# Kernel optimization log

Hardware: AMD Instinct MI355X
Metric: run time of the kernel (lower is better)

## Reference

```python
import jax, jax.numpy as jnp
import numpy as np

N, E, B = 50000, 500000, 32
FEAT, HID, EDGE_DIM = 64, 128, 16
NUM_TASKS, TED, NCLS, TASKS_PER = 5000, 64, 3, 8
NLAYERS = 2


def setup_inputs() -> dict:
    key = jax.random.key(0)
    ks = jax.random.split(key, 20)
    s = 0.05
    inp = {
        "h": jax.random.normal(ks[0], (N, FEAT), jnp.float32),
        "x": jax.random.normal(ks[1], (N, 3), jnp.float32),
        "edge_index": jax.random.randint(ks[2], (2, E), 0, N, dtype=jnp.int32),
        "edge_attr": jax.random.normal(ks[3], (E, EDGE_DIM), jnp.float32),
        "batch": (jnp.arange(N, dtype=jnp.int32) * B // N).astype(jnp.int32),
        "tasks_indices": jnp.stack([
            jnp.repeat(jnp.arange(B, dtype=jnp.int32), TASKS_PER),
            jax.random.randint(ks[4], (B * TASKS_PER,), 0, NUM_TASKS, dtype=jnp.int32),
        ], axis=1),
        "batch_size": B,
        "embed_W": jax.random.normal(ks[5], (FEAT, HID), jnp.float32) * s,
        "embed_b": jnp.zeros((HID,), jnp.float32),
        "res_W": jax.random.normal(ks[6], (NLAYERS, HID, HID), jnp.float32) * s,
        "msg_W": jax.random.normal(ks[7], (NLAYERS, 2 * HID + 1, HID), jnp.float32) * s,
        "msg_b": jnp.zeros((NLAYERS, HID), jnp.float32),
        "upd_W": jax.random.normal(ks[8], (NLAYERS, 2 * HID, HID), jnp.float32) * s,
        "upd_b": jnp.zeros((NLAYERS, HID), jnp.float32),
        "mlp_W0": jax.random.normal(ks[9], (HID + TED, HID), jnp.float32) * s,
        "mlp_b0": jnp.zeros((HID,), jnp.float32),
        "mlp_W1": jax.random.normal(ks[10], (HID, HID), jnp.float32) * s,
        "mlp_b1": jnp.zeros((HID,), jnp.float32),
        "mlp_W2": jax.random.normal(ks[11], (HID, HID), jnp.float32) * s,
        "mlp_b2": jnp.zeros((HID,), jnp.float32),
        "mlp_W3": jax.random.normal(ks[12], (HID, NCLS), jnp.float32) * s,
        "mlp_b3": jnp.zeros((NCLS,), jnp.float32),
        "task_emb": jax.random.normal(ks[13], (NUM_TASKS, TED), jnp.float32),
    }
    return inp


def reference(h, x, edge_index, edge_attr, batch, tasks_indices, batch_size,
              embed_W, embed_b, res_W, msg_W, msg_b, upd_W, upd_b,
              mlp_W0, mlp_b0, mlp_W1, mlp_b1, mlp_W2, mlp_b2, mlp_W3, mlp_b3,
              task_emb):
    n = h.shape[0]
    row, col = edge_index[0], edge_index[1]
    # squared distances, identical across MP layers (positions never updated)
    dist = jnp.sum((x[row] - x[col]) ** 2, axis=1, keepdims=True)  # [E,1]
    emb = h @ embed_W + embed_b  # [N,HID]
    for l in range(NLAYERS):
        msg_in = jnp.concatenate([emb[row], emb[col], dist], axis=-1)  # [E,2H+1]
        msg = jax.nn.relu(msg_in @ msg_W[l] + msg_b[l])                # [E,H]
        aggr = jax.ops.segment_sum(msg, col, num_segments=n)           # [N,H]
        upd = jax.nn.relu(jnp.concatenate([emb, aggr], axis=-1) @ upd_W[l] + upd_b[l])
        emb = emb @ res_W[l] + upd
    # global mean pool per graph
    counts = jax.ops.segment_sum(jnp.ones((n,), emb.dtype), batch, num_segments=batch_size)
    pooled = jax.ops.segment_sum(emb, batch, num_segments=batch_size) / jnp.maximum(counts, 1.0)[:, None]
    # per-(protein, task) head; rows ordered as in the original dict-over-batch loop
    proto = tasks_indices[:, 0]
    tid = tasks_indices[:, 1]
    feat = jnp.concatenate([pooled[proto], task_emb[tid]], axis=-1)  # [K, H+TED]
    z = jax.nn.relu(feat @ mlp_W0 + mlp_b0)
    z = jax.nn.relu(z @ mlp_W1 + mlp_b1)
    z = jax.nn.relu(z @ mlp_W2 + mlp_b2)
    return z @ mlp_W3 + mlp_b3  # [K, NCLS]
```

## Files before the change

### kernel.cpp

```cpp
#include <hip/hip_runtime.h>

constexpr int NN = 50000;
constexpr int NE = 500000;
constexpr int NB = 32;
constexpr int NTROWS = 256;
constexpr int SCB = 196;
constexpr int NBLK64 = (NN + 63) / 64;

typedef __attribute__((ext_vector_type(8))) short bf16x8;
typedef __attribute__((ext_vector_type(4))) float f32x4;

static __device__ __forceinline__ unsigned short f2bf(float f) {
  unsigned u = __float_as_uint(f);
  unsigned r = (u + 0x7FFFu + ((u >> 16) & 1u)) >> 16;
  return (unsigned short)r;
}
static __device__ __forceinline__ float bf2f(unsigned short s) {
  return __uint_as_float(((unsigned)s) << 16);
}

__global__ void k_wprep(const float* __restrict__ msgW, const float* __restrict__ updW,
                        const float* __restrict__ resW, const float* __restrict__ embW,
                        unsigned short* __restrict__ wbf, int* __restrict__ cnt) {
  int idx = blockIdx.x * 256 + threadIdx.x;
  if (idx < NN) cnt[idx] = 0;
  if (idx >= 10 * 16384 + 8192) return;
  if (idx < 10 * 16384) {
    int m = idx >> 14, e = idx & 16383;
    int nn = e >> 7, kk = e & 127;
    int l = m / 5, t = m % 5;
    const float* src;
    if (t == 0)      src = msgW + (size_t)l * 257 * 128;
    else if (t == 1) src = msgW + (size_t)l * 257 * 128 + 128 * 128;
    else if (t == 2) src = updW + (size_t)l * 256 * 128;
    else if (t == 3) src = updW + (size_t)l * 256 * 128 + 128 * 128;
    else             src = resW + (size_t)l * 128 * 128;
    wbf[idx] = f2bf(src[kk * 128 + nn]);
  } else {
    int e = idx - 10 * 16384;
    int nn = e >> 6, kk = e & 63;
    wbf[idx] = f2bf(embW[kk * 128 + nn]);
  }
}

__global__ void k_count_gstart(const int* __restrict__ col, int* __restrict__ cnt,
                               const int* __restrict__ batch, int* __restrict__ gstart) {
  int e = blockIdx.x * 256 + threadIdx.x;
  if (e < NE) atomicAdd(&cnt[col[e]], 1);
  if (e < NN) {
    int b = batch[e];
    if (e == 0) gstart[b] = 0;
    else if (batch[e - 1] != b) gstart[b] = e;
    if (e == NN - 1) gstart[b + 1] = NN;
  }
}

__global__ __launch_bounds__(256) void k_scan1(const int* __restrict__ cnt,
                                               int* __restrict__ starts,
                                               int* __restrict__ bsum) {
  __shared__ int s[256];
  int t = threadIdx.x;
  int i = blockIdx.x * 256 + t;
  int v = (i < NN) ? cnt[i] : 0;
  s[t] = v; __syncthreads();
  for (int off = 1; off < 256; off <<= 1) {
    int u = (t >= off) ? s[t - off] : 0;
    __syncthreads();
    s[t] += u;
    __syncthreads();
  }
  if (i < NN) starts[i] = s[t] - v;
  if (t == 255) bsum[blockIdx.x] = s[255];
}

__global__ __launch_bounds__(256) void k_scan2(int* __restrict__ bsum) {
  __shared__ int s[256];
  int t = threadIdx.x;
  int v = (t < SCB) ? bsum[t] : 0;
  s[t] = v; __syncthreads();
  for (int off = 1; off < 256; off <<= 1) {
    int u = (t >= off) ? s[t - off] : 0;
    __syncthreads();
    s[t] += u;
    __syncthreads();
  }
  if (t < SCB) bsum[t] = s[t] - v;
}

__global__ __launch_bounds__(256) void k_scan3(int* __restrict__ starts,
                                               const int* __restrict__ bsum,
                                               int* __restrict__ cursor) {
  int i = blockIdx.x * 256 + threadIdx.x;
  if (i < NN) {
    int v = starts[i] + bsum[blockIdx.x];
    starts[i] = v;
    cursor[i] = v;
  }
  if (i == 0) starts[NN] = NE;
}

__global__ void k_scatter(const int* __restrict__ row, const int* __restrict__ col,
                          const float* __restrict__ x,
                          int* __restrict__ cursor, int2* __restrict__ spack) {
  int e = blockIdx.x * blockDim.x + threadIdx.x;
  if (e >= NE) return;
  int r = row[e], c = col[e];
  float dx = x[3*r+0] - x[3*c+0];
  float dy = x[3*r+1] - x[3*c+1];
  float dz = x[3*r+2] - x[3*c+2];
  float d = dx*dx + dy*dy + dz*dz;
  int pos = atomicAdd(&cursor[c], 1);
  spack[pos] = make_int2(r, __float_as_int(d));
}

template<int TPB>
static __device__ __forceinline__ void stage_tile64(
    unsigned short* lds, const unsigned short* __restrict__ src, int row0, int n, int tid) {
  #pragma unroll
  for (int ch = tid; ch < 1024; ch += TPB) {
    int r = ch >> 4, kc = ch & 15;
    bf16x8 v = {0,0,0,0,0,0,0,0};
    if (row0 + r < n) v = *(const bf16x8*)(src + (size_t)(row0 + r) * 128 + kc * 8);
    int byte = (r * 256 + kc * 16) ^ ((r & 7) << 4);
    *(bf16x8*)((char*)lds + byte) = v;
  }
}

template<int TPB>
static __device__ __forceinline__ void vstore_tile64(
    unsigned short* __restrict__ dst, const unsigned short* lds, int row0, int n, int tid) {
  #pragma unroll
  for (int ch = tid; ch < 1024; ch += TPB) {
    int r = ch >> 4, kc = ch & 15;
    if (row0 + r < n) {
      bf16x8 v = *(const bf16x8*)((const char*)lds + ((r * 256 + kc * 16) ^ ((r & 7) << 4)));
      *(bf16x8*)(dst + (size_t)(row0 + r) * 128 + kc * 8) = v;
    }
  }
}

static __device__ __forceinline__ void epi_to_lds64(
    unsigned short* lds, const f32x4 (&acc)[4], int lane, int c0) {
  int ccol = lane & 15, crow4 = (lane >> 4) * 4;
  int cc = c0 + ccol;
  #pragma unroll
  for (int rt = 0; rt < 4; ++rt)
    #pragma unroll
    for (int j = 0; j < 4; ++j) {
      int lrow = rt * 16 + crow4 + j;
      int lbyte = (lrow * 256 + cc * 2) ^ ((lrow & 7) << 4);
      *(unsigned short*)((char*)lds + lbyte) = f2bf(acc[rt][j]);
    }
}

static __device__ __forceinline__ void gather_aggr_lds(
    unsigned short* As, const int* __restrict__ starts, const int2* __restrict__ spack,
    const unsigned short* __restrict__ A, const unsigned short* __restrict__ Bm,
    const float* __restrict__ wd, const float* __restrict__ mb,
    int row0, int n, int tid) {
  int c0 = (tid & 15) * 8;
  float4 w0 = *(const float4*)(wd + c0), w1 = *(const float4*)(wd + c0 + 4);
  float4 bb0 = *(const float4*)(mb + c0), bb1 = *(const float4*)(mb + c0 + 4);
  float wv[8] = {w0.x, w0.y, w0.z, w0.w, w1.x, w1.y, w1.z, w1.w};
  float bv[8] = {bb0.x, bb0.y, bb0.z, bb0.w, bb1.x, bb1.y, bb1.z, bb1.w};
  #pragma unroll
  for (int pass = 0; pass < 2; ++pass) {
    int lr = (tid >> 4) + pass * 32;
    int node = row0 + lr;
    union { bf16x8 v; unsigned short s[8]; } o;
    if (node < n) {
      union { bf16x8 v; unsigned short s[8]; } ub;
      ub.v = *(const bf16x8*)(Bm + (size_t)node * 128 + c0);
      float basev[8], accv[8];
      #pragma unroll
      for (int j = 0; j < 8; ++j) { basev[j] = bf2f(ub.s[j]) + bv[j]; accv[j] = 0.f; }
      int s = starts[node], e = starts[node + 1];
      int i = s;
      for (; i + 4 <= e; i += 4) {
        int2 p0 = spack[i + 0], p1 = spack[i + 1];
        int2 p2 = spack[i + 2], p3 = spack[i + 3];
        union { bf16x8 v; unsigned short s[8]; } a0, a1, a2, a3;
        a0.v = *(const bf16x8*)(A + (size_t)p0.x * 128 + c0);
        a1.v = *(const bf16x8*)(A + (size_t)p1.x * 128 + c0);
        a2.v = *(const bf16x8*)(A + (size_t)p2.x * 128 + c0);
        a3.v = *(const bf16x8*)(A + (size_t)p3.x * 128 + c0);
        float d0 = __int_as_float(p0.y), d1 = __int_as_float(p1.y);
        float d2 = __int_as_float(p2.y), d3 = __int_as_float(p3.y);
        #pragma unroll
        for (int j = 0; j < 8; ++j) {
          accv[j] += fmaxf(bf2f(a0.s[j]) + fmaf(d0, wv[j], basev[j]), 0.f);
          accv[j] += fmaxf(bf2f(a1.s[j]) + fmaf(d1, wv[j], basev[j]), 0.f);
          accv[j] += fmaxf(bf2f(a2.s[j]) + fmaf(d2, wv[j], basev[j]), 0.f);
          accv[j] += fmaxf(bf2f(a3.s[j]) + fmaf(d3, wv[j], basev[j]), 0.f);
        }
      }
      for (; i < e; ++i) {
        int2 p = spack[i];
        union { bf16x8 v; unsigned short s[8]; } a;
        a.v = *(const bf16x8*)(A + (size_t)p.x * 128 + c0);
        float d = __int_as_float(p.y);
        #pragma unroll
        for (int j = 0; j < 8; ++j)
          accv[j] += fmaxf(bf2f(a.s[j]) + fmaf(d, wv[j], basev[j]), 0.f);
      }
      #pragma unroll
      for (int j = 0; j < 8; ++j) o.s[j] = f2bf(accv[j]);
    } else {
      #pragma unroll
      for (int j = 0; j < 8; ++j) o.s[j] = 0;
    }
    int byte = (lr * 256 + (tid & 15) * 16) ^ ((lr & 7) << 4);
    *(bf16x8*)((char*)As + byte) = o.v;
  }
}

__global__ __launch_bounds__(512) void k_embed_dual(
    const float* __restrict__ h, const unsigned short* __restrict__ embWt,
    const float* __restrict__ embB,
    const unsigned short* __restrict__ W1t, const unsigned short* __restrict__ W2t,
    unsigned short* __restrict__ emb, unsigned short* __restrict__ Y1,
    unsigned short* __restrict__ Y2, int n) {
  __shared__ unsigned short T0[64 * 128];
  __shared__ unsigned short T1[64 * 128];
  int row0 = blockIdx.x * 64;
  int tid = threadIdx.x;
  int wave = tid >> 6, lane = tid & 63;
  int c0 = wave * 16;
  int arow = lane & 15, kb = (lane >> 4) * 8;
  {
    int r = tid >> 3, kc = tid & 7;
    union { bf16x8 v; unsigned short s[8]; } u;
    if (row0 + r < n) {
      const float* p = h + (size_t)(row0 + r) * 64 + kc * 8;
      float4 f0 = *(const float4*)p, f1 = *(const float4*)(p + 4);
      u.s[0]=f2bf(f0.x); u.s[1]=f2bf(f0.y); u.s[2]=f2bf(f0.z); u.s[3]=f2bf(f0.w);
      u.s[4]=f2bf(f1.x); u.s[5]=f2bf(f1.y); u.s[6]=f2bf(f1.z); u.s[7]=f2bf(f1.w);
    } else {
      #pragma unroll
      for (int j = 0; j < 8; ++j) u.s[j] = 0;
    }
    int byte = (r * 128 + kc * 16) ^ ((r & 7) << 4);
    *(bf16x8*)((char*)T0 + byte) = u.v;
  }
  float bB = embB[c0 + (lane & 15)];
  __syncthreads();
  f32x4 accE[4] = {};
  #pragma unroll
  for (int ks = 0; ks < 2; ++ks) {
    bf16x8 b = *(const bf16x8*)(embWt + (size_t)(c0 + arow) * 64 + ks * 32 + kb);
    #pragma unroll
    for (int rt = 0; rt < 4; ++rt) {
      int r = rt * 16 + arow;
      int byte = (r * 128 + (ks * 32 + kb) * 2) ^ ((r & 7) << 4);
      bf16x8 a = *(const bf16x8*)((const char*)T0 + byte);
      accE[rt] = __builtin_amdgcn_mfma_f32_16x16x32_bf16(a, b, accE[rt], 0, 0, 0);
    }
  }
  {
    int ccol = lane & 15, crow4 = (lane >> 4) * 4;
    int cc = c0 + ccol;
    #pragma unroll
    for (int rt = 0; rt < 4; ++rt)
      #pragma unroll
      for (int j = 0; j < 4; ++j) {
        int lrow = rt * 16 + crow4 + j;
        int lbyte = (lrow * 256 + cc * 2) ^ ((lrow & 7) << 4);
        *(unsigned short*)((char*)T1 + lbyte) = f2bf(accE[rt][j] + bB);
      }
  }
  __syncthreads();
  f32x4 acc1[4] = {};
  f32x4 acc2[4] = {};
  #pragma unroll
  for (int ks = 0; ks < 4; ++ks) {
    int k0 = ks * 32;
    bf16x8 b1 = *(const bf16x8*)(W1t + (size_t)(c0 + arow) * 128 + k0 + kb);
    bf16x8 b2 = *(const bf16x8*)(W2t + (size_t)(c0 + arow) * 128 + k0 + kb);
    #pragma unroll
    for (int rt = 0; rt < 4; ++rt) {
      int r = rt * 16 + arow;
      int byte = (r * 256 + (k0 + kb) * 2) ^ ((r & 7) << 4);
      bf16x8 a = *(const bf16x8*)((const char*)T1 + byte);
      acc1[rt] = __builtin_amdgcn_mfma_f32_16x16x32_bf16(a, b1, acc1[rt], 0, 0, 0);
      acc2[rt] = __builtin_amdgcn_mfma_f32_16x16x32_bf16(a, b2, acc2[rt], 0, 0, 0);
    }
  }
  vstore_tile64<512>(emb, T1, row0, n, tid);
  epi_to_lds64(T0, acc1, lane, c0);
  __syncthreads();
  vstore_tile64<512>(Y1, T0, row0, n, tid);
  __syncthreads();
  epi_to_lds64(T0, acc2, lane, c0);
  __syncthreads();
  vstore_tile64<512>(Y2, T0, row0, n, tid);
}

__global__ __launch_bounds__(512) void k_node_dual_pull(
    const unsigned short* __restrict__ emb,
    const int* __restrict__ starts, const int2* __restrict__ spack,
    const unsigned short* __restrict__ Agth, const unsigned short* __restrict__ Bm,
    const float* __restrict__ wd, const float* __restrict__ mb,
    const unsigned short* __restrict__ U1t, const unsigned short* __restrict__ U2t,
    const unsigned short* __restrict__ Rt, const float* __restrict__ updb,
    const unsigned short* __restrict__ W1t, const unsigned short* __restrict__ W2t,
    unsigned short* __restrict__ out, unsigned short* __restrict__ Y1,
    unsigned short* __restrict__ Y2, int n) {
  __shared__ unsigned short T0[64 * 128];
  __shared__ unsigned short T1[64 * 128];
  int row0 = blockIdx.x * 64;
  int tid = threadIdx.x;
  int wave = tid >> 6, lane = tid & 63;
  int c0 = wave * 16;
  int arow = lane & 15, kb = (lane >> 4) * 8;
  stage_tile64<512>(T0, emb, row0, n, tid);
  gather_aggr_lds(T1, starts, spack, Agth, Bm, wd, mb, row0, n, tid);
  float uB = updb[c0 + (lane & 15)];
  __syncthreads();
  f32x4 accU[4] = {};
  f32x4 accR[4] = {};
  #pragma unroll
  for (int ks = 0; ks < 4; ++ks) {
    int k0 = ks * 32;
    bf16x8 bU1 = *(const bf16x8*)(U1t + (size_t)(c0 + arow) * 128 + k0 + kb);
    bf16x8 bU2 = *(const bf16x8*)(U2t + (size_t)(c0 + arow) * 128 + k0 + kb);
    bf16x8 bR  = *(const bf16x8*)(Rt  + (size_t)(c0 + arow) * 128 + k0 + kb);
    #pragma unroll
    for (int rt = 0; rt < 4; ++rt) {
      int r = rt * 16 + arow;
      int byte = (r * 256 + (k0 + kb) * 2) ^ ((r & 7) << 4);
      bf16x8 aE = *(const bf16x8*)((const char*)T0 + byte);
      bf16x8 aA = *(const bf16x8*)((const char*)T1 + byte);
      accU[rt] = __builtin_amdgcn_mfma_f32_16x16x32_bf16(aE, bU1, accU[rt], 0, 0, 0);
      accU[rt] = __builtin_amdgcn_mfma_f32_16x16x32_bf16(aA, bU2, accU[rt], 0, 0, 0);
      accR[rt] = __builtin_amdgcn_mfma_f32_16x16x32_bf16(aE, bR,  accR[rt], 0, 0, 0);
    }
  }
  __syncthreads();
  {
    int ccol = lane & 15, crow4 = (lane >> 4) * 4;
    int cc = c0 + ccol;
    #pragma unroll
    for (int rt = 0; rt < 4; ++rt)
      #pragma unroll
      for (int j = 0; j < 4; ++j) {
        int lrow = rt * 16 + crow4 + j;
        int lbyte = (lrow * 256 + cc * 2) ^ ((lrow & 7) << 4);
        *(unsigned short*)((char*)T0 + lbyte) =
            f2bf(accR[rt][j] + fmaxf(accU[rt][j] + uB, 0.f));
      }
  }
  __syncthreads();
  f32x4 acc1[4] = {};
  f32x4 acc2[4] = {};
  #pragma unroll
  for (int ks = 0; ks < 4; ++ks) {
    int k0 = ks * 32;
    bf16x8 b1 = *(const bf16x8*)(W1t + (size_t)(c0 + arow) * 128 + k0 + kb);
    bf16x8 b2 = *(const bf16x8*)(W2t + (size_t)(c0 + arow) * 128 + k0 + kb);
    #pragma unroll
    for (int rt = 0; rt < 4; ++rt) {
      int r = rt * 16 + arow;
      int byte = (r * 256 + (k0 + kb) * 2) ^ ((r & 7) << 4);
      bf16x8 a = *(const bf16x8*)((const char*)T0 + byte);
      acc1[rt] = __builtin_amdgcn_mfma_f32_16x16x32_bf16(a, b1, acc1[rt], 0, 0, 0);
      acc2[rt] = __builtin_amdgcn_mfma_f32_16x16x32_bf16(a, b2, acc2[rt], 0, 0, 0);
    }
  }
  vstore_tile64<512>(out, T0, row0, n, tid);
  epi_to_lds64(T1, acc1, lane, c0);
  __syncthreads();
  vstore_tile64<512>(Y1, T1, row0, n, tid);
  __syncthreads();
  epi_to_lds64(T1, acc2, lane, c0);
  __syncthreads();
  vstore_tile64<512>(Y2, T1, row0, n, tid);
}

__global__ __launch_bounds__(512) void k_node_pool_pull(
    const unsigned short* __restrict__ emb,
    const int* __restrict__ starts, const int2* __restrict__ spack,
    const unsigned short* __restrict__ Agth, const unsigned short* __restrict__ Bm,
    const float* __restrict__ wd, const float* __restrict__ mb,
    const unsigned short* __restrict__ U1t, const unsigned short* __restrict__ U2t,
    const unsigned short* __restrict__ Rt, const float* __restrict__ updb,
    const int* __restrict__ batch,
    float* __restrict__ ppart, int* __restrict__ pgid, int n) {
  __shared__ unsigned short Es[64 * 128];
  __shared__ unsigned short As[64 * 128];
  __shared__ int sbat[64];
  int row0 = blockIdx.x * 64;
  int tid = threadIdx.x;
  int wave = tid >> 6, lane = tid & 63;
  int c0 = wave * 16;
  int arow = lane & 15, kb = (lane >> 4) * 8;
  stage_tile64<512>(Es, emb, row0, n, tid);
  if (tid < 64) sbat[tid] = batch[min(row0 + tid, n - 1)];
  gather_aggr_lds(As, starts, spack, Agth, Bm, wd, mb, row0, n, tid);
  float uB = updb[c0 + (lane & 15)];
  __syncthreads();
  f32x4 accU[4] = {};
  f32x4 accR[4] = {};
  #pragma unroll
  for (int ks = 0; ks < 4; ++ks) {
    int k0 = ks * 32;
    bf16x8 bU1 = *(const bf16x8*)(U1t + (size_t)(c0 + arow) * 128 + k0 + kb);
    bf16x8 bU2 = *(const bf16x8*)(U2t + (size_t)(c0 + arow) * 128 + k0 + kb);
    bf16x8 bR  = *(const bf16x8*)(Rt  + (size_t)(c0 + arow) * 128 + k0 + kb);
    #pragma unroll
    for (int rt = 0; rt < 4; ++rt) {
      int r = rt * 16 + arow;
      int byte = (r * 256 + (k0 + kb) * 2) ^ ((r & 7) << 4);
      bf16x8 aE = *(const bf16x8*)((const char*)Es + byte);
      bf16x8 aA = *(const bf16x8*)((const char*)As + byte);
      accU[rt] = __builtin_amdgcn_mfma_f32_16x16x32_bf16(aE, bU1, accU[rt], 0, 0, 0);
      accU[rt] = __builtin_amdgcn_mfma_f32_16x16x32_bf16(aA, bU2, accU[rt], 0, 0, 0);
      accR[rt] = __builtin_amdgcn_mfma_f32_16x16x32_bf16(aE, bR,  accR[rt], 0, 0, 0);
    }
  }
  int g0 = sbat[0];
  int crow4 = (lane >> 4) * 4;
  float s0 = 0.f, s1 = 0.f;
  #pragma unroll
  for (int rt = 0; rt < 4; ++rt)
    #pragma unroll
    for (int j = 0; j < 4; ++j) {
      int lrow = rt * 16 + crow4 + j;
      if (row0 + lrow < n) {
        float v = accR[rt][j] + fmaxf(accU[rt][j] + uB, 0.f);
        if (sbat[lrow] == g0) s0 += v; else s1 += v;
      }
    }
  s0 += __shfl_xor(s0, 16); s0 += __shfl_xor(s0, 32);
  s1 += __shfl_xor(s1, 16); s1 += __shfl_xor(s1, 32);
  if ((lane >> 4) == 0) {
    int cc = c0 + (lane & 15);
    ppart[(size_t)(2 * blockIdx.x) * 128 + cc] = s0;
    ppart[(size_t)(2 * blockIdx.x + 1) * 128 + cc] = s1;
  }
  if (tid == 0) {
    int gl = sbat[63];
    pgid[2 * blockIdx.x] = g0;
    pgid[2 * blockIdx.x + 1] = (gl != g0) ? gl : -1;
  }
}

__global__ __launch_bounds__(128) void k_pool2(const float* __restrict__ ppart,
                                               const int* __restrict__ pgid,
                                               const int* __restrict__ gstart,
                                               float* __restrict__ pooled) {
  int g = blockIdx.x, t = threadIdx.x;
  int blo = gstart[g] >> 6;
  int bhi = (gstart[g + 1] - 1) >> 6;
  float acc = 0.f;
  for (int b = blo; b <= bhi; ++b) {
    if (pgid[2 * b] == g)     acc += ppart[(size_t)(2 * b) * 128 + t];
    if (pgid[2 * b + 1] == g) acc += ppart[(size_t)(2 * b + 1) * 128 + t];
  }
  float cntf = (float)(gstart[g + 1] - gstart[g]);
  pooled[g * 128 + t] = acc / fmaxf(cntf, 1.f);
}

__global__ __launch_bounds__(128) void k_head(
    const float* __restrict__ pooled, const float* __restrict__ temb,
    const int* __restrict__ tasks,
    const float* __restrict__ W0, const float* __restrict__ b0,
    const float* __restrict__ W1, const float* __restrict__ b1,
    const float* __restrict__ W2, const float* __restrict__ b2,
    const float* __restrict__ W3, const float* __restrict__ b3,
    float* __restrict__ out) {
  __shared__ float f[192];
  __shared__ float za[128];
  __shared__ float zb[128];
  int rowi = blockIdx.x, t = threadIdx.x;
  int proto = tasks[rowi*2 + 0];
  int tid2  = tasks[rowi*2 + 1];
  f[t] = pooled[proto*128 + t];
  if (t < 64) f[128 + t] = temb[(size_t)tid2*64 + t];
  __syncthreads();
  float a = b0[t];
  for (int k = 0; k < 192; ++k) a += f[k] * W0[k*128 + t];
  za[t] = fmaxf(a, 0.f);
  __syncthreads();
  a = b1[t];
  for (int k = 0; k < 128; ++k) a += za[k] * W1[k*128 + t];
  zb[t] = fmaxf(a, 0.f);
  __syncthreads();
  a = b2[t];
  for (int k = 0; k < 128; ++k) a += zb[k] * W2[k*128 + t];
  za[t] = fmaxf(a, 0.f);
  __syncthreads();
  if (t < 3) {
    a = b3[t];
    for (int k = 0; k < 128; ++k) a += za[k] * W3[k*3 + t];
    out[rowi*3 + t] = a;
  }
}

extern "C" void kernel_launch(void* const* d_in, const int* in_sizes, int n_in,
                              void* d_out, int out_size, void* d_ws, size_t ws_size,
                              hipStream_t stream) {
  const float* h    = (const float*)d_in[0];
  const float* x    = (const float*)d_in[1];
  const int*   ei   = (const int*)d_in[2];
  const int*   batch= (const int*)d_in[4];
  const int*   tasks= (const int*)d_in[5];
  const float* embW = (const float*)d_in[7];
  const float* embB = (const float*)d_in[8];
  const float* resW = (const float*)d_in[9];
  const float* msgW = (const float*)d_in[10];
  const float* msgB = (const float*)d_in[11];
  const float* updW = (const float*)d_in[12];
  const float* updB = (const float*)d_in[13];
  const float* W0 = (const float*)d_in[14]; const float* b0 = (const float*)d_in[15];
  const float* W1 = (const float*)d_in[16]; const float* b1 = (const float*)d_in[17];
  const float* W2 = (const float*)d_in[18]; const float* b2 = (const float*)d_in[19];
  const float* W3 = (const float*)d_in[20]; const float* b3 = (const float*)d_in[21];
  const float* temb = (const float*)d_in[22];
  const int* row = ei;
  const int* col = ei + NE;

  unsigned short* bws = (unsigned short*)d_ws;
  unsigned short* e0   = bws;  bws += (size_t)NN*128;
  unsigned short* e1   = bws;  bws += (size_t)NN*128;
  unsigned short* A0   = bws;  bws += (size_t)NN*128;
  unsigned short* B0   = bws;  bws += (size_t)NN*128;
  unsigned short* A1   = bws;  bws += (size_t)NN*128;
  unsigned short* B1   = bws;  bws += (size_t)NN*128;
  unsigned short* wbf  = bws;  bws += 10*16384 + 8192;
  float* ws = (float*)bws;
  float* pooled= ws;  ws += NB*128;
  float* ppart = ws;  ws += (size_t)2*NBLK64*128;
  int2*  spack = (int2*)ws;
  int*   iws   = (int*)(spack + NE);
  int*   cnt    = iws;  iws += NN;
  int*   starts = iws;  iws += NN + 1;
  int*   cursor = iws;  iws += NN;
  int*   gstart = iws;  iws += NB + 1;
  int*   bsum   = iws;  iws += 256;
  int*   pgid   = iws;  iws += 2*NBLK64;

  const unsigned short* embWt = wbf + (size_t)10*16384;

  k_wprep<<<672, 256, 0, stream>>>(msgW, updW, resW, embW, wbf, cnt);

  k_count_gstart<<<(NE + 255)/256, 256, 0, stream>>>(col, cnt, batch, gstart);
  k_scan1<<<SCB, 256, 0, stream>>>(cnt, starts, bsum);
  k_scan2<<<1, 256, 0, stream>>>(bsum);
  k_scan3<<<SCB, 256, 0, stream>>>(starts, bsum, cursor);
  k_scatter<<<(NE + 255)/256, 256, 0, stream>>>(row, col, x, cursor, spack);

  const unsigned short* m0W1t = wbf + (size_t)0 * 16384;
  const unsigned short* m0W2t = wbf + (size_t)1 * 16384;
  const unsigned short* u0W1t = wbf + (size_t)2 * 16384;
  const unsigned short* u0W2t = wbf + (size_t)3 * 16384;
  const unsigned short* r0Wt  = wbf + (size_t)4 * 16384;
  const unsigned short* m1W1t = wbf + (size_t)5 * 16384;
  const unsigned short* m1W2t = wbf + (size_t)6 * 16384;
  const unsigned short* u1W1t = wbf + (size_t)7 * 16384;
  const unsigned short* u1W2t = wbf + (size_t)8 * 16384;
  const unsigned short* r1Wt  = wbf + (size_t)9 * 16384;

  k_embed_dual<<<NBLK64, 512, 0, stream>>>(h, embWt, embB, m0W1t, m0W2t,
                                           e0, A0, B0, NN);
  k_node_dual_pull<<<NBLK64, 512, 0, stream>>>(e0, starts, spack, A0, B0,
                                               msgW + 256*128, msgB,
                                               u0W1t, u0W2t, r0Wt, updB,
                                               m1W1t, m1W2t, e1, A1, B1, NN);
  k_node_pool_pull<<<NBLK64, 512, 0, stream>>>(e1, starts, spack, A1, B1,
                                               msgW + (size_t)257*128 + 256*128,
                                               msgB + 128,
                                               u1W1t, u1W2t, r1Wt, updB + 128,
                                               batch, ppart, pgid, NN);
  k_pool2<<<NB, 128, 0, stream>>>(ppart, pgid, gstart, pooled);
  k_head<<<NTROWS, 128, 0, stream>>>(pooled, temb, tasks,
                                     W0, b0, W1, b1, W2, b2, W3, b3, (float*)d_out);
}
```

Before: 206.7 us.

## Merge small preprocessing kernels and fuse pooling into head to cut launches

Several small kernel launches are merged into combined grids. Weight prep joins edge counting, the second and third scan phases are replaced by a per-block reduction, edge scatter shares a launch with the embed GEMM, and pooling is folded into the head kernel. The cnt zeroing moves to a memset, and launch_bounds gain a min-blocks hint for the pull kernels. This removes launch overhead and serialization gaps, at the cost of redundant per-block reductions, recomputing the pool for each head row, and possible register pressure from the occupancy hint.

```diff
diff --git a/kernel.cpp b/kernel.cpp
--- a/kernel.cpp
+++ b/kernel.cpp
@@ -6,6 +6,7 @@
 constexpr int NTROWS = 256;
 constexpr int SCB = 196;
 constexpr int NBLK64 = (NN + 63) / 64;
+constexpr int SCAT_BLK = (NE + 511) / 512;
 
 typedef __attribute__((ext_vector_type(8))) short bf16x8;
 typedef __attribute__((ext_vector_type(4))) float f32x4;
@@ -19,39 +20,39 @@
   return __uint_as_float(((unsigned)s) << 16);
 }
 
-__global__ void k_wprep(const float* __restrict__ msgW, const float* __restrict__ updW,
-                        const float* __restrict__ resW, const float* __restrict__ embW,
-                        unsigned short* __restrict__ wbf, int* __restrict__ cnt) {
-  int idx = blockIdx.x * 256 + threadIdx.x;
-  if (idx < NN) cnt[idx] = 0;
-  if (idx >= 10 * 16384 + 8192) return;
-  if (idx < 10 * 16384) {
-    int m = idx >> 14, e = idx & 16383;
-    int nn = e >> 7, kk = e & 127;
-    int l = m / 5, t = m % 5;
-    const float* src;
-    if (t == 0)      src = msgW + (size_t)l * 257 * 128;
-    else if (t == 1) src = msgW + (size_t)l * 257 * 128 + 128 * 128;
-    else if (t == 2) src = updW + (size_t)l * 256 * 128;
-    else if (t == 3) src = updW + (size_t)l * 256 * 128 + 128 * 128;
-    else             src = resW + (size_t)l * 128 * 128;
-    wbf[idx] = f2bf(src[kk * 128 + nn]);
+__global__ void k_prep_count(const float* __restrict__ msgW, const float* __restrict__ updW,
+                             const float* __restrict__ resW, const float* __restrict__ embW,
+                             unsigned short* __restrict__ wbf,
+                             const int* __restrict__ col, int* __restrict__ cnt,
+                             const int* __restrict__ batch, int* __restrict__ gstart) {
+  if (blockIdx.x < 672) {
+    int idx = blockIdx.x * 256 + threadIdx.x;
+    if (idx >= 10 * 16384 + 8192) return;
+    if (idx < 10 * 16384) {
+      int m = idx >> 14, e = idx & 16383;
+      int nn = e >> 7, kk = e & 127;
+      int l = m / 5, t = m % 5;
+      const float* src;
+      if (t == 0)      src = msgW + (size_t)l * 257 * 128;
+      else if (t == 1) src = msgW + (size_t)l * 257 * 128 + 128 * 128;
+      else if (t == 2) src = updW + (size_t)l * 256 * 128;
+      else if (t == 3) src = updW + (size_t)l * 256 * 128 + 128 * 128;
+      else             src = resW + (size_t)l * 128 * 128;
+      wbf[idx] = f2bf(src[kk * 128 + nn]);
+    } else {
+      int e = idx - 10 * 16384;
+      int nn = e >> 6, kk = e & 63;
+      wbf[idx] = f2bf(embW[kk * 128 + nn]);
+    }
   } else {
-    int e = idx - 10 * 16384;
-    int nn = e >> 6, kk = e & 63;
-    wbf[idx] = f2bf(embW[kk * 128 + nn]);
-  }
-}
-
-__global__ void k_count_gstart(const int* __restrict__ col, int* __restrict__ cnt,
-                               const int* __restrict__ batch, int* __restrict__ gstart) {
-  int e = blockIdx.x * 256 + threadIdx.x;
-  if (e < NE) atomicAdd(&cnt[col[e]], 1);
-  if (e < NN) {
-    int b = batch[e];
-    if (e == 0) gstart[b] = 0;
-    else if (batch[e - 1] != b) gstart[b] = e;
-    if (e == NN - 1) gstart[b + 1] = NN;
+    int e = (blockIdx.x - 672) * 256 + threadIdx.x;
+    if (e < NE) atomicAdd(&cnt[col[e]], 1);
+    if (e < NN) {
+      int b = batch[e];
+      if (e == 0) gstart[b] = 0;
+      else if (batch[e - 1] != b) gstart[b] = e;
+      if (e == NN - 1) gstart[b + 1] = NN;
+    }
   }
 }
 
@@ -73,44 +74,26 @@
   if (t == 255) bsum[blockIdx.x] = s[255];
 }
 
-__global__ __launch_bounds__(256) void k_scan2(int* __restrict__ bsum) {
-  __shared__ int s[256];
+__global__ __launch_bounds__(256) void k_scan3b(int* __restrict__ starts,
+                                                const int* __restrict__ bsum,
+                                                int* __restrict__ cursor) {
+  __shared__ int red[256];
   int t = threadIdx.x;
-  int v = (t < SCB) ? bsum[t] : 0;
-  s[t] = v; __syncthreads();
-  for (int off = 1; off < 256; off <<= 1) {
-    int u = (t >= off) ? s[t - off] : 0;
+  red[t] = (t < (int)blockIdx.x && t < SCB) ? bsum[t] : 0;
+  __syncthreads();
+  #pragma unroll
+  for (int s = 128; s > 0; s >>= 1) {
+    if (t < s) red[t] += red[t + s];
     __syncthreads();
-    s[t] += u;
-    __syncthreads();
-  }
-  if (t < SCB) bsum[t] = s[t] - v;
-}
-
-__global__ __launch_bounds__(256) void k_scan3(int* __restrict__ starts,
-                                               const int* __restrict__ bsum,
-                                               int* __restrict__ cursor) {
-  int i = blockIdx.x * 256 + threadIdx.x;
+  }
+  int off = red[0];
+  int i = blockIdx.x * 256 + t;
   if (i < NN) {
-    int v = starts[i] + bsum[blockIdx.x];
+    int v = starts[i] + off;
     starts[i] = v;
     cursor[i] = v;
   }
   if (i == 0) starts[NN] = NE;
-}
-
-__global__ void k_scatter(const int* __restrict__ row, const int* __restrict__ col,
-                          const float* __restrict__ x,
-                          int* __restrict__ cursor, int2* __restrict__ spack) {
-  int e = blockIdx.x * blockDim.x + threadIdx.x;
-  if (e >= NE) return;
-  int r = row[e], c = col[e];
-  float dx = x[3*r+0] - x[3*c+0];
-  float dy = x[3*r+1] - x[3*c+1];
-  float dz = x[3*r+2] - x[3*c+2];
-  float d = dx*dx + dy*dy + dz*dz;
-  int pos = atomicAdd(&cursor[c], 1);
-  spack[pos] = make_int2(r, __float_as_int(d));
 }
 
 template<int TPB>
@@ -214,16 +197,31 @@
   }
 }
 
-__global__ __launch_bounds__(512) void k_embed_dual(
+__global__ __launch_bounds__(512) void k_scatter_embed(
     const float* __restrict__ h, const unsigned short* __restrict__ embWt,
     const float* __restrict__ embB,
     const unsigned short* __restrict__ W1t, const unsigned short* __restrict__ W2t,
     unsigned short* __restrict__ emb, unsigned short* __restrict__ Y1,
-    unsigned short* __restrict__ Y2, int n) {
+    unsigned short* __restrict__ Y2, int n,
+    const int* __restrict__ row, const int* __restrict__ col,
+    const float* __restrict__ x, int* __restrict__ cursor, int2* __restrict__ spack) {
   __shared__ unsigned short T0[64 * 128];
   __shared__ unsigned short T1[64 * 128];
+  int tid = threadIdx.x;
+  if (blockIdx.x >= NBLK64) {
+    int e = (blockIdx.x - NBLK64) * 512 + tid;
+    if (e < NE) {
+      int r = row[e], c = col[e];
+      float dx = x[3*r+0] - x[3*c+0];
+      float dy = x[3*r+1] - x[3*c+1];
+      float dz = x[3*r+2] - x[3*c+2];
+      float d = dx*dx + dy*dy + dz*dz;
+      int pos = atomicAdd(&cursor[c], 1);
+      spack[pos] = make_int2(r, __float_as_int(d));
+    }
+    return;
+  }
   int row0 = blockIdx.x * 64;
-  int tid = threadIdx.x;
   int wave = tid >> 6, lane = tid & 63;
   int c0 = wave * 16;
   int arow = lane & 15, kb = (lane >> 4) * 8;
@@ -295,7 +293,7 @@
   vstore_tile64<512>(Y2, T0, row0, n, tid);
 }
 
-__global__ __launch_bounds__(512) void k_node_dual_pull(
+__global__ __launch_bounds__(512, 4) void k_node_dual_pull(
     const unsigned short* __restrict__ emb,
     const int* __restrict__ starts, const int2* __restrict__ spack,
     const unsigned short* __restrict__ Agth, const unsigned short* __restrict__ Bm,
@@ -376,7 +374,7 @@
   vstore_tile64<512>(Y2, T1, row0, n, tid);
 }
 
-__global__ __launch_bounds__(512) void k_node_pool_pull(
+__global__ __launch_bounds__(512, 4) void k_node_pool_pull(
     const unsigned short* __restrict__ emb,
     const int* __restrict__ starts, const int2* __restrict__ spack,
     const unsigned short* __restrict__ Agth, const unsigned short* __restrict__ Bm,
@@ -444,25 +442,10 @@
   }
 }
 
-__global__ __launch_bounds__(128) void k_pool2(const float* __restrict__ ppart,
-                                               const int* __restrict__ pgid,
-                                               const int* __restrict__ gstart,
-                                               float* __restrict__ pooled) {
-  int g = blockIdx.x, t = threadIdx.x;
-  int blo = gstart[g] >> 6;
-  int bhi = (gstart[g + 1] - 1) >> 6;
-  float acc = 0.f;
-  for (int b = blo; b <= bhi; ++b) {
-    if (pgid[2 * b] == g)     acc += ppart[(size_t)(2 * b) * 128 + t];
-    if (pgid[2 * b + 1] == g) acc += ppart[(size_t)(2 * b + 1) * 128 + t];
-  }
-  float cntf = (float)(gstart[g + 1] - gstart[g]);
-  pooled[g * 128 + t] = acc / fmaxf(cntf, 1.f);
-}
-
-__global__ __launch_bounds__(128) void k_head(
-    const float* __restrict__ pooled, const float* __restrict__ temb,
-    const int* __restrict__ tasks,
+__global__ __launch_bounds__(128) void k_pool_head(
+    const float* __restrict__ ppart, const int* __restrict__ pgid,
+    const int* __restrict__ gstart,
+    const float* __restrict__ temb, const int* __restrict__ tasks,
     const float* __restrict__ W0, const float* __restrict__ b0,
     const float* __restrict__ W1, const float* __restrict__ b1,
     const float* __restrict__ W2, const float* __restrict__ b2,
@@ -474,7 +457,17 @@
   int rowi = blockIdx.x, t = threadIdx.x;
   int proto = tasks[rowi*2 + 0];
   int tid2  = tasks[rowi*2 + 1];
-  f[t] = pooled[proto*128 + t];
+  {
+    int blo = gstart[proto] >> 6;
+    int bhi = (gstart[proto + 1] - 1) >> 6;
+    float acc = 0.f;
+    for (int b = blo; b <= bhi; ++b) {
+      if (pgid[2 * b] == proto)     acc += ppart[(size_t)(2 * b) * 128 + t];
+      if (pgid[2 * b + 1] == proto) acc += ppart[(size_t)(2 * b + 1) * 128 + t];
+    }
+    float cntf = (float)(gstart[proto + 1] - gstart[proto]);
+    f[t] = acc / fmaxf(cntf, 1.f);
+  }
   if (t < 64) f[128 + t] = temb[(size_t)tid2*64 + t];
   __syncthreads();
   float a = b0[t];
@@ -528,7 +521,6 @@
   unsigned short* B1   = bws;  bws += (size_t)NN*128;
   unsigned short* wbf  = bws;  bws += 10*16384 + 8192;
   float* ws = (float*)bws;
-  float* pooled= ws;  ws += NB*128;
   float* ppart = ws;  ws += (size_t)2*NBLK64*128;
   int2*  spack = (int2*)ws;
   int*   iws   = (int*)(spack + NE);
@@ -540,14 +532,6 @@
   int*   pgid   = iws;  iws += 2*NBLK64;
 
   const unsigned short* embWt = wbf + (size_t)10*16384;
-
-  k_wprep<<<672, 256, 0, stream>>>(msgW, updW, resW, embW, wbf, cnt);
-
-  k_count_gstart<<<(NE + 255)/256, 256, 0, stream>>>(col, cnt, batch, gstart);
-  k_scan1<<<SCB, 256, 0, stream>>>(cnt, starts, bsum);
-  k_scan2<<<1, 256, 0, stream>>>(bsum);
-  k_scan3<<<SCB, 256, 0, stream>>>(starts, bsum, cursor);
-  k_scatter<<<(NE + 255)/256, 256, 0, stream>>>(row, col, x, cursor, spack);
 
   const unsigned short* m0W1t = wbf + (size_t)0 * 16384;
   const unsigned short* m0W2t = wbf + (size_t)1 * 16384;
@@ -560,8 +544,14 @@
   const unsigned short* u1W2t = wbf + (size_t)8 * 16384;
   const unsigned short* r1Wt  = wbf + (size_t)9 * 16384;
 
-  k_embed_dual<<<NBLK64, 512, 0, stream>>>(h, embWt, embB, m0W1t, m0W2t,
-                                           e0, A0, B0, NN);
+  hipMemsetAsync(cnt, 0, NN * sizeof(int), stream);
+  k_prep_count<<<672 + (NE + 255)/256, 256, 0, stream>>>(msgW, updW, resW, embW, wbf,
+                                                         col, cnt, batch, gstart);
+  k_scan1<<<SCB, 256, 0, stream>>>(cnt, starts, bsum);
+  k_scan3b<<<SCB, 256, 0, stream>>>(starts, bsum, cursor);
+  k_scatter_embed<<<NBLK64 + SCAT_BLK, 512, 0, stream>>>(h, embWt, embB, m0W1t, m0W2t,
+                                                         e0, A0, B0, NN,
+                                                         row, col, x, cursor, spack);
   k_node_dual_pull<<<NBLK64, 512, 0, stream>>>(e0, starts, spack, A0, B0,
                                                msgW + 256*128, msgB,
                                                u0W1t, u0W2t, r0Wt, updB,
@@ -571,7 +561,6 @@
                                                msgB + 128,
                                                u1W1t, u1W2t, r1Wt, updB + 128,
                                                batch, ppart, pgid, NN);
-  k_pool2<<<NB, 128, 0, stream>>>(ppart, pgid, gstart, pooled);
-  k_head<<<NTROWS, 128, 0, stream>>>(pooled, temb, tasks,
-                                     W0, b0, W1, b1, W2, b2, W3, b3, (float*)d_out);
-}
+  k_pool_head<<<NTROWS, 128, 0, stream>>>(ppart, pgid, gstart, temb, tasks,
+                                          W0, b0, W1, b1, W2, b2, W3, b3, (float*)d_out);
+}
```

After: 196.5 us. 1.05x faster.
